# Kernel optimization log

Hardware: AMD Instinct MI355X
Metric: run time of the kernel (lower is better)

## Reference

```python
import jax, jax.numpy as jnp
import numpy as np

B, S, HID = 2, 2048, 2048
NH, NKV, HD = 16, 8, 128
GROUPS = NH // NKV
EPS = 1e-6
SCALE = HD ** -0.5
ROPE_THETA = 1000000.0


def _rope_cos_sin(seq_len, head_dim, batch):
    inv_freq = 1.0 / (ROPE_THETA ** (np.arange(0, head_dim, 2, dtype=np.float32) / head_dim))
    t = np.arange(seq_len, dtype=np.float32)
    freqs = np.outer(t, inv_freq)                      # [S, HD/2]
    emb = np.concatenate([freqs, freqs], axis=-1)      # [S, HD]
    cos = np.broadcast_to(np.cos(emb), (batch, seq_len, head_dim))
    sin = np.broadcast_to(np.sin(emb), (batch, seq_len, head_dim))
    return jnp.asarray(cos), jnp.asarray(sin)


def setup_inputs() -> dict:
    key = jax.random.key(0)
    ks = jax.random.split(key, 6)
    hidden_states = jax.random.normal(ks[0], (B, S, HID), dtype=jnp.float32)
    cos, sin = _rope_cos_sin(S, HD, B)
    w_scale = HID ** -0.5
    Wq = jax.random.normal(ks[1], (NH * HD, HID), dtype=jnp.float32) * w_scale
    Wk = jax.random.normal(ks[2], (NKV * HD, HID), dtype=jnp.float32) * w_scale
    Wv = jax.random.normal(ks[3], (NKV * HD, HID), dtype=jnp.float32) * w_scale
    Wo = jax.random.normal(ks[4], (HID, NH * HD), dtype=jnp.float32) * w_scale
    q_norm_w = jnp.ones((HD,), dtype=jnp.float32)
    k_norm_w = jnp.ones((HD,), dtype=jnp.float32)
    return {"hidden_states": hidden_states, "cos": cos, "sin": sin,
            "Wq": Wq, "Wk": Wk, "Wv": Wv, "Wo": Wo,
            "q_norm_w": q_norm_w, "k_norm_w": k_norm_w}


def _rms_norm(x, w):
    # RMSNorm over last dim (head_dim), variance computed in fp32
    var = jnp.mean(x.astype(jnp.float32) ** 2, axis=-1, keepdims=True)
    return w * (x * jax.lax.rsqrt(var + EPS).astype(x.dtype))


def _rotate_half(x):
    x1, x2 = jnp.split(x, 2, axis=-1)
    return jnp.concatenate([-x2, x1], axis=-1)


def _apply_rope(x, cos, sin):
    # x: [B, H, S, D]; cos/sin: [B, S, D] -> unsqueeze head dim
    c = cos[:, None, :, :]
    s = sin[:, None, :, :]
    return x * c + _rotate_half(x) * s


def reference(hidden_states, cos, sin, Wq, Wk, Wv, Wo, q_norm_w, k_norm_w):
    b, s, _ = hidden_states.shape
    # QKV projections (bias=False per config.attention_bias)
    q = (hidden_states @ Wq.T).reshape(b, s, NH, HD)
    k = (hidden_states @ Wk.T).reshape(b, s, NKV, HD)
    v = (hidden_states @ Wv.T).reshape(b, s, NKV, HD)
    # Per-head QK RMSNorm, then [B, H, S, D]
    q = _rms_norm(q, q_norm_w).transpose(0, 2, 1, 3)
    k = _rms_norm(k, k_norm_w).transpose(0, 2, 1, 3)
    v = v.transpose(0, 2, 1, 3)
    # RoPE
    q = _apply_rope(q, cos, sin)
    k = _apply_rope(k, cos, sin)
    # GQA: expand kv heads to match query heads
    k = jnp.repeat(k, GROUPS, axis=1)
    v = jnp.repeat(v, GROUPS, axis=1)
    # SDPA (is_causal=False, mask=None, dropout=0)
    scores = jnp.einsum('bhqd,bhkd->bhqk', q, k) * SCALE
    probs = jax.nn.softmax(scores, axis=-1)
    attn = jnp.einsum('bhqk,bhkd->bhqd', probs, v)
    attn = attn.transpose(0, 2, 1, 3).reshape(b, s, NH * HD)
    return attn @ Wo.T
```

## Files before the change

kernel.cpp:

```cpp
#include <hip/hip_runtime.h>

using short8 = __attribute__((ext_vector_type(8))) short;
using f32x4  = __attribute__((ext_vector_type(4))) float;
using u32x2  = __attribute__((ext_vector_type(2))) unsigned int;
using u32x4  = __attribute__((ext_vector_type(4))) unsigned int;

#define MFMA16(a, b, c) __builtin_amdgcn_mfma_f32_16x16x32_bf16((a), (b), (c), 0, 0, 0)

__device__ inline float bf2f(ushort v) { return __uint_as_float(((unsigned int)v) << 16); }
__device__ inline unsigned int f2bfu(float f) {
  unsigned int u = __float_as_uint(f);
  return (u + 0x7fffu + ((u >> 16) & 1u)) >> 16;
}
__device__ inline unsigned int pk2(float a, float b) { return f2bfu(a) | (f2bfu(b) << 16); }

__device__ inline void gl_lds16(const ushort* g, ushort* l) {
  __builtin_amdgcn_global_load_lds(
      (const __attribute__((address_space(1))) void*)g,
      (__attribute__((address_space(3))) void*)l, 16, 0, 0);
}

__global__ __launch_bounds__(256) void f2b8(const float* __restrict__ src,
                                            ushort* __restrict__ dst, int n) {
  int i = (blockIdx.x * 256 + threadIdx.x) * 8;
  if (i >= n) return;
  f32x4 a = *(const f32x4*)(src + i);
  f32x4 b = *(const f32x4*)(src + i + 4);
  u32x4 o;
  o[0] = pk2(a[0], a[1]); o[1] = pk2(a[2], a[3]);
  o[2] = pk2(b[0], b[1]); o[3] = pk2(b[2], b[3]);
  *(u32x4*)(dst + i) = o;
}

#define GPHASE(CB, P, STG, VMW)                                                     \
  {                                                                                 \
    if (P == 0) {                                                                   \
      _Pragma("unroll") for (int n = 0; n < 4; ++n) {                               \
        bf[n][0] = *(const short8*)&L[(CB)*32768 + bBase + n*1024 + rdoff];         \
        bf[n][1] = *(const short8*)&L[(CB)*32768 + bBase + n*1024 + (rdoff ^ 32)];  \
      }                                                                             \
    }                                                                               \
    short8 af[2][2];                                                                \
    _Pragma("unroll") for (int mi = 0; mi < 2; ++mi) {                              \
      af[mi][0] = *(const short8*)&L[(CB)*32768 + aBase + ((P)*2+mi)*1024 + rdoff];        \
      af[mi][1] = *(const short8*)&L[(CB)*32768 + aBase + ((P)*2+mi)*1024 + (rdoff ^ 32)]; \
    }                                                                               \
    STG;                                                                            \
    __builtin_amdgcn_s_barrier();                                                   \
    asm volatile("s_waitcnt lgkmcnt(0)" ::: "memory");                              \
    __builtin_amdgcn_s_setprio(1);                                                  \
    _Pragma("unroll") for (int mi = 0; mi < 2; ++mi)                                \
      _Pragma("unroll") for (int n = 0; n < 4; ++n) {                               \
        acc[(P)*2+mi][n] = MFMA16(af[mi][0], bf[n][0], acc[(P)*2+mi][n]);           \
        acc[(P)*2+mi][n] = MFMA16(af[mi][1], bf[n][1], acc[(P)*2+mi][n]);           \
      }                                                                             \
    __builtin_amdgcn_s_setprio(0);                                                  \
    VMW;                                                                            \
    __builtin_amdgcn_s_barrier();                                                   \
  }

#define VM4 asm volatile("s_waitcnt vmcnt(4)" ::: "memory")
#define NOPX (void)0

template <int OUTF32>
__global__ __launch_bounds__(512, 2) void gemm256(const ushort* __restrict__ A,
                                                  const ushort* __restrict__ B,
                                                  void* __restrict__ Cv,
                                                  int M, int N, int K) {
  __shared__ ushort L[65536];
  const int t = threadIdx.x;
  const int w = t >> 6, l = t & 63, lr = l & 15, lg = l >> 4;
  const int wr = w >> 2, wc = w & 3;
  const int m0 = blockIdx.x * 256, n0 = blockIdx.y * 256;
  const int NT = K >> 6, NI = NT >> 1;

  f32x4 acc[8][4] = {};

  const int rdoff = lr * 64 + ((lg ^ (lr & 7)) * 8);
  const int aBase = wr * 8192;
  const int bBase = 16384 + (wc >> 1) * 8192 + (wc & 1) * 4096;

  const int ch0 = w * 2, ch1 = w * 2 + 1;
  const int srow0 = ch0 * 8 + (l >> 3), srow1 = ch1 * 8 + (l >> 3);
  const int scol = ((l & 7) ^ (l >> 3)) * 8;

  auto stage_a = [&](int h, int kt, int cb) {
    int ktc = kt < NT ? kt : NT - 1;
    gl_lds16(A + (size_t)(m0 + h * 128 + srow0) * K + ktc * 64 + scol,
             (ushort*)&L[cb * 32768 + h * 8192 + ch0 * 512]);
    gl_lds16(A + (size_t)(m0 + h * 128 + srow1) * K + ktc * 64 + scol,
             (ushort*)&L[cb * 32768 + h * 8192 + ch1 * 512]);
  };
  auto stage_b = [&](int h, int kt, int cb) {
    int ktc = kt < NT ? kt : NT - 1;
    gl_lds16(B + (size_t)(n0 + h * 128 + srow0) * K + ktc * 64 + scol,
             (ushort*)&L[cb * 32768 + 16384 + h * 8192 + ch0 * 512]);
    gl_lds16(B + (size_t)(n0 + h * 128 + srow1) * K + ktc * 64 + scol,
             (ushort*)&L[cb * 32768 + 16384 + h * 8192 + ch1 * 512]);
  };

  stage_a(0, 0, 0); stage_a(1, 0, 0); stage_b(0, 0, 0); stage_b(1, 0, 0);
  stage_b(0, 1, 1); stage_b(1, 1, 1);
  VM4;
  __builtin_amdgcn_s_barrier();

  short8 bf[4][2];
  for (int I = 0; I < NI; ++I) {
    const int t1 = 2 * I + 1, t2 = 2 * I + 2, t3 = 2 * I + 3;
    GPHASE(0, 0, stage_a(0, t1, 1), NOPX)
    GPHASE(0, 1, stage_a(1, t1, 1), NOPX)
    GPHASE(0, 2, stage_b(0, t2, 0), NOPX)
    GPHASE(0, 3, stage_b(1, t2, 0), VM4)
    GPHASE(1, 0, stage_a(0, t2, 0), NOPX)
    GPHASE(1, 1, stage_a(1, t2, 0), NOPX)
    GPHASE(1, 2, stage_b(0, t3, 1), NOPX)
    GPHASE(1, 3, stage_b(1, t3, 1), VM4)
  }

  const int crow0 = m0 + wr * 128 + lg * 4;
  const int ccol = n0 + wc * 64 + lr;
  if (OUTF32) {
    float* C = (float*)Cv;
#pragma unroll
    for (int m = 0; m < 8; ++m)
#pragma unroll
      for (int n = 0; n < 4; ++n)
#pragma unroll
        for (int j = 0; j < 4; ++j)
          C[(size_t)(crow0 + m * 16 + j) * N + ccol + n * 16] = acc[m][n][j];
  } else {
    ushort* C = (ushort*)Cv;
#pragma unroll
    for (int m = 0; m < 8; ++m)
#pragma unroll
      for (int n = 0; n < 4; ++n)
#pragma unroll
        for (int j = 0; j < 4; ++j)
          C[(size_t)(crow0 + m * 16 + j) * N + ccol + n * 16] = (ushort)f2bfu(acc[m][n][j]);
  }
}

__global__ __launch_bounds__(256) void qk_norm_rope(
    const ushort* __restrict__ QKVp, const float* __restrict__ cosb,
    const float* __restrict__ sinb, const float* __restrict__ qw,
    const float* __restrict__ kw, ushort* __restrict__ Qa, ushort* __restrict__ Ka) {
  int r = blockIdx.x * 4 + (threadIdx.x >> 6);
  int i = threadIdx.x & 63;
  int b, s, srccol;
  ushort* dst;
  const float* w;
  float scale;
  if (r < 65536) {
    b = r >> 15; int rem = r & 32767; s = rem >> 4; int h = rem & 15;
    srccol = h * 128;
    dst = Qa + ((size_t)((b * 16 + h) * 2048 + s)) * 128;
    w = qw;
    scale = 0.08838834764831845f * 1.4426950408889634f;
  } else {
    int rk = r - 65536;
    b = rk >> 14; int rem = rk & 16383; s = rem >> 3; int kvh = rem & 7;
    srccol = 2048 + kvh * 128;
    dst = Ka + ((size_t)((b * 8 + kvh) * 2048 + s)) * 128;
    w = kw;
    scale = 1.0f;
  }
  const ushort* src = QKVp + ((size_t)(b * 2048 + s)) * 4096 + srccol;
  float x0 = bf2f(src[i]), x1 = bf2f(src[i + 64]);
  float ss = x0 * x0 + x1 * x1;
#pragma unroll
  for (int m = 1; m < 64; m <<= 1) ss += __shfl_xor(ss, m);
  float inv = rsqrtf(ss * (1.0f / 128.0f) + 1e-6f);
  float xn0 = x0 * inv * w[i], xn1 = x1 * inv * w[i + 64];
  const float* cp = cosb + ((size_t)(b * 2048 + s)) * 128;
  const float* sp = sinb + ((size_t)(b * 2048 + s)) * 128;
  float o0 = (xn0 * cp[i] - xn1 * sp[i]) * scale;
  float o1 = (xn1 * cp[i + 64] + xn0 * sp[i + 64]) * scale;
  dst[i] = (ushort)f2bfu(o0);
  dst[i + 64] = (ushort)f2bfu(o1);
}

__global__ __launch_bounds__(256) void v_transpose(const ushort* __restrict__ QKVp,
                                                   ushort* __restrict__ Vt) {
  __shared__ ushort tile[64][136];
  int blk = blockIdx.x;
  int st = blk & 31, kvh = (blk >> 5) & 7, b = blk >> 8;
  int t = threadIdx.x;
  int s0 = st * 64;
  {
    int r = t >> 2, cseg = (t & 3) * 32;
    const ushort* src = QKVp + ((size_t)(b * 2048 + s0 + r)) * 4096 + 3072 + kvh * 128 + cseg;
#pragma unroll
    for (int i = 0; i < 4; ++i)
      *(uint4*)&tile[r][cseg + i * 8] = *(const uint4*)(src + i * 8);
  }
  __syncthreads();
  {
    int d = t >> 1, sh = (t & 1) * 32;
    ushort* dst = Vt + ((size_t)((b * 8 + kvh) * 128 + d)) * 2048 + s0 + sh;
    ushort buf[32];
#pragma unroll
    for (int k = 0; k < 32; ++k) buf[k] = tile[sh + k][d];
#pragma unroll
    for (int i = 0; i < 4; ++i) *(uint4*)(dst + i * 8) = *(uint4*)&buf[i * 8];
  }
}

__global__ __launch_bounds__(256, 2) void attn_kernel(const ushort* __restrict__ Qa,
                                                      const ushort* __restrict__ Ka,
                                                      const ushort* __restrict__ Vt,
                                                      ushort* __restrict__ Ctx) {
  __shared__ ushort Ks[2][64 * 128];
  __shared__ ushort Vs[2][128 * 64];
  __shared__ ushort Ps[8 * 1024];
  const int bh = blockIdx.x, b = bh >> 4, h = bh & 15, kvh = h >> 1;
  const int t = threadIdx.x, w = t >> 6, l = t & 63, lr = l & 15, lg = l >> 4;
  const int q0 = blockIdx.y * 128 + w * 32;
  const ushort* Qh = Qa + ((size_t)(b * 16 + h)) * 2048 * 128;
  const ushort* Kh = Ka + ((size_t)(b * 8 + kvh)) * 2048 * 128;
  const ushort* Vh = Vt + ((size_t)(b * 8 + kvh)) * 128 * 2048;

  short8 bq[2][4];
#pragma unroll
  for (int qt = 0; qt < 2; ++qt)
#pragma unroll
    for (int dc = 0; dc < 4; ++dc)
      bq[qt][dc] = *(const short8*)&Qh[(size_t)(q0 + qt * 16 + lr) * 128 + dc * 32 + lg * 8];
  asm volatile("s_waitcnt vmcnt(0)" ::: "memory");

  f32x4 accO[8][2] = {};
  float mrun[2] = {-3.0e38f, -3.0e38f};
  float lrun[2] = {0.f, 0.f};

  auto stage = [&](int kt0, ushort* KSB, ushort* VSB) {
#pragma unroll
    for (int i = 0; i < 4; ++i) {
      const int c = w * 4 + i;
      const int krow = c * 4 + lg;
      gl_lds16(Kh + (size_t)(kt0 + krow) * 128 + (((l & 15) ^ (krow & 7)) * 8),
               KSB + c * 512);
      const int vrow = c * 8 + (l >> 3);
      gl_lds16(Vh + (size_t)vrow * 2048 + kt0 + (((l & 7) ^ ((l >> 3) & 7)) * 8),
               VSB + c * 512);
    }
  };

  auto iter = [&](int kt, const ushort* KSB, const ushort* VSB, ushort* KSN, ushort* VSN) {
    f32x4 accS[4][2] = {};
#pragma unroll
    for (int dc = 0; dc < 4; ++dc) {
      short8 ak[4];
#pragma unroll
      for (int kts = 0; kts < 4; ++kts)
        ak[kts] = *(const short8*)&KSB[(kts * 16 + lr) * 128 + ((dc * 4 + lg) ^ (lr & 7)) * 8];
#pragma unroll
      for (int kts = 0; kts < 4; ++kts)
#pragma unroll
        for (int qt = 0; qt < 2; ++qt)
          accS[kts][qt] = MFMA16(ak[kts], bq[qt][dc], accS[kts][qt]);
    }

#pragma unroll
    for (int qt = 0; qt < 2; ++qt) {
      float m0 = fmaxf(fmaxf(accS[0][qt][0], accS[0][qt][1]), fmaxf(accS[0][qt][2], accS[0][qt][3]));
      float m1 = fmaxf(fmaxf(accS[1][qt][0], accS[1][qt][1]), fmaxf(accS[1][qt][2], accS[1][qt][3]));
      float m2 = fmaxf(fmaxf(accS[2][qt][0], accS[2][qt][1]), fmaxf(accS[2][qt][2], accS[2][qt][3]));
      float m3 = fmaxf(fmaxf(accS[3][qt][0], accS[3][qt][1]), fmaxf(accS[3][qt][2], accS[3][qt][3]));
      float tm = fmaxf(fmaxf(m0, m1), fmaxf(m2, m3));
      tm = fmaxf(tm, __shfl_xor(tm, 16));
      tm = fmaxf(tm, __shfl_xor(tm, 32));
      if (!__all(tm <= mrun[qt] + 11.0f)) {
        float nm = fmaxf(mrun[qt], tm);
        float cf = __builtin_amdgcn_exp2f(mrun[qt] - nm);
#pragma unroll
        for (int dc = 0; dc < 8; ++dc) {
          accO[dc][qt][0] *= cf; accO[dc][qt][1] *= cf;
          accO[dc][qt][2] *= cf; accO[dc][qt][3] *= cf;
        }
        lrun[qt] *= cf;
        mrun[qt] = nm;
      }
      float ts = 0.f;
#pragma unroll
      for (int kts = 0; kts < 4; ++kts)
#pragma unroll
        for (int j = 0; j < 4; ++j) {
          float p = __builtin_amdgcn_exp2f(accS[kts][qt][j] - mrun[qt]);
          accS[kts][qt][j] = p;
          ts += p;
        }
      ts += __shfl_xor(ts, 16);
      ts += __shfl_xor(ts, 32);
      lrun[qt] += ts;
#pragma unroll
      for (int kts = 0; kts < 4; ++kts) {
        u32x2 pv;
        pv[0] = pk2(accS[kts][qt][0], accS[kts][qt][1]);
        pv[1] = pk2(accS[kts][qt][2], accS[kts][qt][3]);
        *(u32x2*)&Ps[(w * 2 + qt) * 1024 + lr * 64 +
                     (((kts * 2 + (lg >> 1)) ^ (lr & 7)) * 8 + (lg & 1) * 4)] = pv;
      }
    }
    asm volatile("s_waitcnt lgkmcnt(0)" ::: "memory");

    short8 bp[2][2];
#pragma unroll
    for (int qt = 0; qt < 2; ++qt)
#pragma unroll
      for (int ks = 0; ks < 2; ++ks)
        bp[qt][ks] = *(const short8*)&Ps[(w * 2 + qt) * 1024 + lr * 64 +
                                         ((ks * 4 + lg) ^ (lr & 7)) * 8];
#pragma unroll
    for (int dc = 0; dc < 8; ++dc) {
      short8 av[2];
#pragma unroll
      for (int ks = 0; ks < 2; ++ks)
        av[ks] = *(const short8*)&VSB[(dc * 16 + lr) * 64 + ((ks * 4 + lg) ^ (lr & 7)) * 8];
#pragma unroll
      for (int ks = 0; ks < 2; ++ks)
#pragma unroll
        for (int qt = 0; qt < 2; ++qt)
          accO[dc][qt] = MFMA16(av[ks], bp[qt][ks], accO[dc][qt]);
    }

    asm volatile("" ::: "memory");
    __builtin_amdgcn_s_barrier();
    if (kt + 128 <= 2048) {
      stage(kt + 128, KSN, VSN);
      asm volatile("s_waitcnt vmcnt(8)" ::: "memory");
    } else {
      asm volatile("s_waitcnt vmcnt(0)" ::: "memory");
    }
    __builtin_amdgcn_s_barrier();
  };

  stage(0, Ks[0], Vs[0]);
  stage(64, Ks[1], Vs[1]);
  asm volatile("s_waitcnt vmcnt(8)" ::: "memory");
  __builtin_amdgcn_s_barrier();

  for (int t2 = 0; t2 < 2048; t2 += 128) {
    iter(t2,      Ks[0], Vs[0], Ks[0], Vs[0]);
    iter(t2 + 64, Ks[1], Vs[1], Ks[1], Vs[1]);
  }

#pragma unroll
  for (int qt = 0; qt < 2; ++qt) {
    float inv = 1.0f / lrun[qt];
    int srow = q0 + qt * 16 + lr;
#pragma unroll
    for (int dc = 0; dc < 8; ++dc) {
      u32x2 ov;
      ov[0] = pk2(accO[dc][qt][0] * inv, accO[dc][qt][1] * inv);
      ov[1] = pk2(accO[dc][qt][2] * inv, accO[dc][qt][3] * inv);
      *(u32x2*)&Ctx[(size_t)(b * 2048 + srow) * 2048 + h * 128 + dc * 16 + lg * 4] = ov;
    }
  }
}

extern "C" void kernel_launch(void* const* d_in, const int* in_sizes, int n_in,
                              void* d_out, int out_size, void* d_ws, size_t ws_size,
                              hipStream_t stream) {
  const float* hidden = (const float*)d_in[0];
  const float* cosb   = (const float*)d_in[1];
  const float* sinb   = (const float*)d_in[2];
  const float* Wq     = (const float*)d_in[3];
  const float* Wk     = (const float*)d_in[4];
  const float* Wv     = (const float*)d_in[5];
  const float* Wo     = (const float*)d_in[6];
  const float* qw     = (const float*)d_in[7];
  const float* kw     = (const float*)d_in[8];

  char* ws = (char*)d_ws;
  ushort* Xb    = (ushort*)ws; ws += (size_t)4096 * 2048 * 2;
  ushort* Wcomb = (ushort*)ws; ws += (size_t)4096 * 2048 * 2;
  ushort* Wob   = (ushort*)ws; ws += (size_t)2048 * 2048 * 2;
  ushort* QKVp  = (ushort*)ws; ws += (size_t)4096 * 4096 * 2;
  ushort* Qa    = (ushort*)ws; ws += (size_t)2 * 16 * 2048 * 128 * 2;
  ushort* Ka    = (ushort*)ws; ws += (size_t)2 * 8 * 2048 * 128 * 2;
  ushort* Vt    = (ushort*)ws; ws += (size_t)2 * 8 * 2048 * 128 * 2;
  ushort* Ctx   = (ushort*)ws; ws += (size_t)4096 * 2048 * 2;

  f2b8<<<4096, 256, 0, stream>>>(hidden, Xb, 8388608);
  f2b8<<<2048, 256, 0, stream>>>(Wq, Wcomb, 4194304);
  f2b8<<<1024, 256, 0, stream>>>(Wk, Wcomb + 4194304, 2097152);
  f2b8<<<1024, 256, 0, stream>>>(Wv, Wcomb + 6291456, 2097152);
  f2b8<<<2048, 256, 0, stream>>>(Wo, Wob, 4194304);

  gemm256<0><<<dim3(16, 16), 512, 0, stream>>>(Xb, Wcomb, (void*)QKVp, 4096, 4096, 2048);

  qk_norm_rope<<<24576, 256, 0, stream>>>(QKVp, cosb, sinb, qw, kw, Qa, Ka);
  v_transpose<<<512, 256, 0, stream>>>(QKVp, Vt);

  attn_kernel<<<dim3(32, 16), 256, 0, stream>>>(Qa, Ka, Vt, Ctx);

  gemm256<1><<<dim3(16, 8), 512, 0, stream>>>(Ctx, Wob, d_out, 4096, 2048, 2048);
}
```

Before: 362.3 us.

## Retile attention to 8 waves, add 128-row output GEMM, fuse weight casts

The attention kernel now runs 512 threads per block, with each wave owning 16 query rows instead of 32. It also uses s_setprio around its MFMA sections and packs bf16 with the hardware v_cvt_pk_bf16_f32 instruction. A new gemm128 kernel with 128x256 tiles replaces the 256-tile output projection, doubling the grid to fill more CUs. The four weight-conversion launches are merged into one kernel. Together these aim to raise occupancy, improve CU utilisation on the output GEMM, and cut launch overhead, at the cost of more K/V LDS traffic per query row.

After: 358.8 us. About the same (-1.0%).

```diff
diff --git a/kernel.cpp b/kernel.cpp
--- a/kernel.cpp
+++ b/kernel.cpp
@@ -13,6 +13,11 @@
   return (u + 0x7fffu + ((u >> 16) & 1u)) >> 16;
 }
 __device__ inline unsigned int pk2(float a, float b) { return f2bfu(a) | (f2bfu(b) << 16); }
+__device__ inline unsigned int pk2hw(float lo, float hi) {
+  unsigned int r;
+  asm("v_cvt_pk_bf16_f32 %0, %1, %2" : "=v"(r) : "v"(lo), "v"(hi));
+  return r;
+}
 
 __device__ inline void gl_lds16(const ushort* g, ushort* l) {
   __builtin_amdgcn_global_load_lds(
@@ -24,6 +29,27 @@
                                             ushort* __restrict__ dst, int n) {
   int i = (blockIdx.x * 256 + threadIdx.x) * 8;
   if (i >= n) return;
+  f32x4 a = *(const f32x4*)(src + i);
+  f32x4 b = *(const f32x4*)(src + i + 4);
+  u32x4 o;
+  o[0] = pk2(a[0], a[1]); o[1] = pk2(a[2], a[3]);
+  o[2] = pk2(b[0], b[1]); o[3] = pk2(b[2], b[3]);
+  *(u32x4*)(dst + i) = o;
+}
+
+__global__ __launch_bounds__(256) void wconv(const float* __restrict__ Wq,
+                                             const float* __restrict__ Wk,
+                                             const float* __restrict__ Wv,
+                                             const float* __restrict__ Wo,
+                                             ushort* __restrict__ Wcomb,
+                                             ushort* __restrict__ Wob) {
+  int blk = blockIdx.x;
+  const float* src; ushort* dst; int off;
+  if (blk < 2048)      { src = Wq; dst = Wcomb;           off = blk * 2048; }
+  else if (blk < 3072) { src = Wk; dst = Wcomb + 4194304; off = (blk - 2048) * 2048; }
+  else if (blk < 4096) { src = Wv; dst = Wcomb + 6291456; off = (blk - 3072) * 2048; }
+  else                 { src = Wo; dst = Wob;             off = (blk - 4096) * 2048; }
+  int i = off + threadIdx.x * 8;
   f32x4 a = *(const f32x4*)(src + i);
   f32x4 b = *(const f32x4*)(src + i + 4);
   u32x4 o;
@@ -140,6 +166,92 @@
   }
 }
 
+#define GP128(CB, P, STG, VMW)                                                      \
+  {                                                                                 \
+    if (P == 0) {                                                                   \
+      _Pragma("unroll") for (int n = 0; n < 4; ++n) {                               \
+        bf[n][0] = *(const short8*)&L[(CB)*24576 + bBase + n*1024 + rdoff];         \
+        bf[n][1] = *(const short8*)&L[(CB)*24576 + bBase + n*1024 + (rdoff ^ 32)];  \
+      }                                                                             \
+    }                                                                               \
+    short8 af0 = *(const short8*)&L[(CB)*24576 + aBase + (P)*1024 + rdoff];         \
+    short8 af1 = *(const short8*)&L[(CB)*24576 + aBase + (P)*1024 + (rdoff ^ 32)];  \
+    STG;                                                                            \
+    __builtin_amdgcn_s_barrier();                                                   \
+    asm volatile("s_waitcnt lgkmcnt(0)" ::: "memory");                              \
+    __builtin_amdgcn_s_setprio(1);                                                  \
+    _Pragma("unroll") for (int n = 0; n < 4; ++n) {                                 \
+      acc[(P)][n] = MFMA16(af0, bf[n][0], acc[(P)][n]);                             \
+      acc[(P)][n] = MFMA16(af1, bf[n][1], acc[(P)][n]);                             \
+    }                                                                               \
+    __builtin_amdgcn_s_setprio(0);                                                  \
+    VMW;                                                                            \
+    __builtin_amdgcn_s_barrier();                                                   \
+  }
+
+__global__ __launch_bounds__(512, 2) void gemm128(const ushort* __restrict__ A,
+                                                  const ushort* __restrict__ B,
+                                                  float* __restrict__ C,
+                                                  int M, int N, int K) {
+  __shared__ ushort L[49152];
+  const int t = threadIdx.x;
+  const int w = t >> 6, l = t & 63, lr = l & 15, lg = l >> 4;
+  const int wr = w >> 2, wc = w & 3;
+  const int m0 = blockIdx.x * 128, n0 = blockIdx.y * 256;
+  const int NT = K >> 6, NI = NT >> 1;
+
+  f32x4 acc[4][4] = {};
+
+  const int rdoff = lr * 64 + ((lg ^ (lr & 7)) * 8);
+  const int aBase = wr * 4096;
+  const int bBase = 8192 + wc * 4096;
+  const int scol = ((l & 7) ^ (l >> 3)) * 8;
+
+  auto stage_a_h = [&](int h, int kt, int cb) {
+    int ktc = kt < NT ? kt : NT - 1;
+    int ch = h * 8 + w;
+    gl_lds16(A + (size_t)(m0 + ch * 8 + (l >> 3)) * K + ktc * 64 + scol,
+             (ushort*)&L[cb * 24576 + ch * 512]);
+  };
+  auto stage_b_h = [&](int h, int kt, int cb) {
+    int ktc = kt < NT ? kt : NT - 1;
+    int c0 = h * 16 + w * 2, c1 = c0 + 1;
+    gl_lds16(B + (size_t)(n0 + c0 * 8 + (l >> 3)) * K + ktc * 64 + scol,
+             (ushort*)&L[cb * 24576 + 8192 + c0 * 512]);
+    gl_lds16(B + (size_t)(n0 + c1 * 8 + (l >> 3)) * K + ktc * 64 + scol,
+             (ushort*)&L[cb * 24576 + 8192 + c1 * 512]);
+  };
+
+  stage_a_h(0, 0, 0); stage_a_h(1, 0, 0);
+  stage_b_h(0, 0, 0); stage_b_h(1, 0, 0);
+  stage_b_h(0, 1, 1); stage_b_h(1, 1, 1);
+  VM4;
+  __builtin_amdgcn_s_barrier();
+
+  short8 bf[4][2];
+  for (int I = 0; I < NI; ++I) {
+    const int t1 = 2 * I + 1, t2 = 2 * I + 2, t3 = 2 * I + 3;
+    GP128(0, 0, stage_a_h(0, t1, 1), NOPX)
+    GP128(0, 1, stage_a_h(1, t1, 1), NOPX)
+    GP128(0, 2, stage_b_h(0, t2, 0), NOPX)
+    GP128(0, 3, stage_b_h(1, t2, 0), VM4)
+    GP128(1, 0, stage_a_h(0, t2, 0), NOPX)
+    GP128(1, 1, stage_a_h(1, t2, 0), NOPX)
+    GP128(1, 2, stage_b_h(0, t3, 1), NOPX)
+    GP128(1, 3, stage_b_h(1, t3, 1), VM4)
+  }
+
+  const int crow0 = m0 + wr * 64 + lg * 4;
+  const int ccol = n0 + wc * 64 + lr;
+#pragma unroll
+  for (int m = 0; m < 4; ++m)
+#pragma unroll
+    for (int n = 0; n < 4; ++n)
+#pragma unroll
+      for (int j = 0; j < 4; ++j)
+        C[(size_t)(crow0 + m * 16 + j) * N + ccol + n * 16] = acc[m][n][j];
+}
+
 __global__ __launch_bounds__(256) void qk_norm_rope(
     const ushort* __restrict__ QKVp, const float* __restrict__ cosb,
     const float* __restrict__ sinb, const float* __restrict__ qw,
@@ -205,7 +317,7 @@
   }
 }
 
-__global__ __launch_bounds__(256, 2) void attn_kernel(const ushort* __restrict__ Qa,
+__global__ __launch_bounds__(512, 4) void attn_kernel(const ushort* __restrict__ Qa,
                                                       const ushort* __restrict__ Ka,
                                                       const ushort* __restrict__ Vt,
                                                       ushort* __restrict__ Ctx) {
@@ -214,38 +326,34 @@
   __shared__ ushort Ps[8 * 1024];
   const int bh = blockIdx.x, b = bh >> 4, h = bh & 15, kvh = h >> 1;
   const int t = threadIdx.x, w = t >> 6, l = t & 63, lr = l & 15, lg = l >> 4;
-  const int q0 = blockIdx.y * 128 + w * 32;
+  const int q0 = blockIdx.y * 128 + w * 16;
   const ushort* Qh = Qa + ((size_t)(b * 16 + h)) * 2048 * 128;
   const ushort* Kh = Ka + ((size_t)(b * 8 + kvh)) * 2048 * 128;
   const ushort* Vh = Vt + ((size_t)(b * 8 + kvh)) * 128 * 2048;
 
-  short8 bq[2][4];
-#pragma unroll
-  for (int qt = 0; qt < 2; ++qt)
-#pragma unroll
-    for (int dc = 0; dc < 4; ++dc)
-      bq[qt][dc] = *(const short8*)&Qh[(size_t)(q0 + qt * 16 + lr) * 128 + dc * 32 + lg * 8];
+  short8 bq[4];
+#pragma unroll
+  for (int dc = 0; dc < 4; ++dc)
+    bq[dc] = *(const short8*)&Qh[(size_t)(q0 + lr) * 128 + dc * 32 + lg * 8];
   asm volatile("s_waitcnt vmcnt(0)" ::: "memory");
 
-  f32x4 accO[8][2] = {};
-  float mrun[2] = {-3.0e38f, -3.0e38f};
-  float lrun[2] = {0.f, 0.f};
+  f32x4 accO[8] = {};
+  float mrun = -3.0e38f, lrun = 0.f;
 
   auto stage = [&](int kt0, ushort* KSB, ushort* VSB) {
 #pragma unroll
-    for (int i = 0; i < 4; ++i) {
-      const int c = w * 4 + i;
+    for (int i = 0; i < 2; ++i) {
+      const int c = w * 2 + i;
       const int krow = c * 4 + lg;
-      gl_lds16(Kh + (size_t)(kt0 + krow) * 128 + (((l & 15) ^ (krow & 7)) * 8),
-               KSB + c * 512);
+      gl_lds16(Kh + (size_t)(kt0 + krow) * 128 + ((lr ^ (krow & 7)) * 8), KSB + c * 512);
       const int vrow = c * 8 + (l >> 3);
-      gl_lds16(Vh + (size_t)vrow * 2048 + kt0 + (((l & 7) ^ ((l >> 3) & 7)) * 8),
-               VSB + c * 512);
-    }
-  };
-
-  auto iter = [&](int kt, const ushort* KSB, const ushort* VSB, ushort* KSN, ushort* VSN) {
-    f32x4 accS[4][2] = {};
+      gl_lds16(Vh + (size_t)vrow * 2048 + kt0 + (((l & 7) ^ ((l >> 3) & 7)) * 8), VSB + c * 512);
+    }
+  };
+
+  auto iter = [&](int kt, ushort* KSB, ushort* VSB) {
+    f32x4 accS[4] = {};
+    __builtin_amdgcn_s_setprio(1);
 #pragma unroll
     for (int dc = 0; dc < 4; ++dc) {
       short8 ak[4];
@@ -254,61 +362,57 @@
         ak[kts] = *(const short8*)&KSB[(kts * 16 + lr) * 128 + ((dc * 4 + lg) ^ (lr & 7)) * 8];
 #pragma unroll
       for (int kts = 0; kts < 4; ++kts)
-#pragma unroll
-        for (int qt = 0; qt < 2; ++qt)
-          accS[kts][qt] = MFMA16(ak[kts], bq[qt][dc], accS[kts][qt]);
-    }
-
-#pragma unroll
-    for (int qt = 0; qt < 2; ++qt) {
-      float m0 = fmaxf(fmaxf(accS[0][qt][0], accS[0][qt][1]), fmaxf(accS[0][qt][2], accS[0][qt][3]));
-      float m1 = fmaxf(fmaxf(accS[1][qt][0], accS[1][qt][1]), fmaxf(accS[1][qt][2], accS[1][qt][3]));
-      float m2 = fmaxf(fmaxf(accS[2][qt][0], accS[2][qt][1]), fmaxf(accS[2][qt][2], accS[2][qt][3]));
-      float m3 = fmaxf(fmaxf(accS[3][qt][0], accS[3][qt][1]), fmaxf(accS[3][qt][2], accS[3][qt][3]));
+        accS[kts] = MFMA16(ak[kts], bq[dc], accS[kts]);
+    }
+    __builtin_amdgcn_s_setprio(0);
+
+    {
+      float m0 = fmaxf(fmaxf(accS[0][0], accS[0][1]), fmaxf(accS[0][2], accS[0][3]));
+      float m1 = fmaxf(fmaxf(accS[1][0], accS[1][1]), fmaxf(accS[1][2], accS[1][3]));
+      float m2 = fmaxf(fmaxf(accS[2][0], accS[2][1]), fmaxf(accS[2][2], accS[2][3]));
+      float m3 = fmaxf(fmaxf(accS[3][0], accS[3][1]), fmaxf(accS[3][2], accS[3][3]));
       float tm = fmaxf(fmaxf(m0, m1), fmaxf(m2, m3));
       tm = fmaxf(tm, __shfl_xor(tm, 16));
       tm = fmaxf(tm, __shfl_xor(tm, 32));
-      if (!__all(tm <= mrun[qt] + 11.0f)) {
-        float nm = fmaxf(mrun[qt], tm);
-        float cf = __builtin_amdgcn_exp2f(mrun[qt] - nm);
+      if (!__all(tm <= mrun + 11.0f)) {
+        float nm = fmaxf(mrun, tm);
+        float cf = __builtin_amdgcn_exp2f(mrun - nm);
 #pragma unroll
         for (int dc = 0; dc < 8; ++dc) {
-          accO[dc][qt][0] *= cf; accO[dc][qt][1] *= cf;
-          accO[dc][qt][2] *= cf; accO[dc][qt][3] *= cf;
+          accO[dc][0] *= cf; accO[dc][1] *= cf;
+          accO[dc][2] *= cf; accO[dc][3] *= cf;
         }
-        lrun[qt] *= cf;
-        mrun[qt] = nm;
+        lrun *= cf;
+        mrun = nm;
       }
       float ts = 0.f;
 #pragma unroll
       for (int kts = 0; kts < 4; ++kts)
 #pragma unroll
         for (int j = 0; j < 4; ++j) {
-          float p = __builtin_amdgcn_exp2f(accS[kts][qt][j] - mrun[qt]);
-          accS[kts][qt][j] = p;
+          float p = __builtin_amdgcn_exp2f(accS[kts][j] - mrun);
+          accS[kts][j] = p;
           ts += p;
         }
       ts += __shfl_xor(ts, 16);
       ts += __shfl_xor(ts, 32);
-      lrun[qt] += ts;
+      lrun += ts;
 #pragma unroll
       for (int kts = 0; kts < 4; ++kts) {
         u32x2 pv;
-        pv[0] = pk2(accS[kts][qt][0], accS[kts][qt][1]);
-        pv[1] = pk2(accS[kts][qt][2], accS[kts][qt][3]);
-        *(u32x2*)&Ps[(w * 2 + qt) * 1024 + lr * 64 +
+        pv[0] = pk2hw(accS[kts][0], accS[kts][1]);
+        pv[1] = pk2hw(accS[kts][2], accS[kts][3]);
+        *(u32x2*)&Ps[w * 1024 + lr * 64 +
                      (((kts * 2 + (lg >> 1)) ^ (lr & 7)) * 8 + (lg & 1) * 4)] = pv;
       }
     }
     asm volatile("s_waitcnt lgkmcnt(0)" ::: "memory");
 
-    short8 bp[2][2];
-#pragma unroll
-    for (int qt = 0; qt < 2; ++qt)
-#pragma unroll
-      for (int ks = 0; ks < 2; ++ks)
-        bp[qt][ks] = *(const short8*)&Ps[(w * 2 + qt) * 1024 + lr * 64 +
-                                         ((ks * 4 + lg) ^ (lr & 7)) * 8];
+    short8 bp[2];
+#pragma unroll
+    for (int ks = 0; ks < 2; ++ks)
+      bp[ks] = *(const short8*)&Ps[w * 1024 + lr * 64 + ((ks * 4 + lg) ^ (lr & 7)) * 8];
+    __builtin_amdgcn_s_setprio(1);
 #pragma unroll
     for (int dc = 0; dc < 8; ++dc) {
       short8 av[2];
@@ -317,16 +421,15 @@
         av[ks] = *(const short8*)&VSB[(dc * 16 + lr) * 64 + ((ks * 4 + lg) ^ (lr & 7)) * 8];
 #pragma unroll
       for (int ks = 0; ks < 2; ++ks)
-#pragma unroll
-        for (int qt = 0; qt < 2; ++qt)
-          accO[dc][qt] = MFMA16(av[ks], bp[qt][ks], accO[dc][qt]);
-    }
+        accO[dc] = MFMA16(av[ks], bp[ks], accO[dc]);
+    }
+    __builtin_amdgcn_s_setprio(0);
 
     asm volatile("" ::: "memory");
     __builtin_amdgcn_s_barrier();
-    if (kt + 128 <= 2048) {
-      stage(kt + 128, KSN, VSN);
-      asm volatile("s_waitcnt vmcnt(8)" ::: "memory");
+    if (kt + 128 < 2048) {
+      stage(kt + 128, KSB, VSB);
+      asm volatile("s_waitcnt vmcnt(4)" ::: "memory");
     } else {
       asm volatile("s_waitcnt vmcnt(0)" ::: "memory");
     }
@@ -335,23 +438,22 @@
 
   stage(0, Ks[0], Vs[0]);
   stage(64, Ks[1], Vs[1]);
-  asm volatile("s_waitcnt vmcnt(8)" ::: "memory");
+  asm volatile("s_waitcnt vmcnt(4)" ::: "memory");
   __builtin_amdgcn_s_barrier();
 
   for (int t2 = 0; t2 < 2048; t2 += 128) {
-    iter(t2,      Ks[0], Vs[0], Ks[0], Vs[0]);
-    iter(t2 + 64, Ks[1], Vs[1], Ks[1], Vs[1]);
-  }
-
-#pragma unroll
-  for (int qt = 0; qt < 2; ++qt) {
-    float inv = 1.0f / lrun[qt];
-    int srow = q0 + qt * 16 + lr;
+    iter(t2,      Ks[0], Vs[0]);
+    iter(t2 + 64, Ks[1], Vs[1]);
+  }
+
+  {
+    float inv = 1.0f / lrun;
+    int srow = q0 + lr;
 #pragma unroll
     for (int dc = 0; dc < 8; ++dc) {
       u32x2 ov;
-      ov[0] = pk2(accO[dc][qt][0] * inv, accO[dc][qt][1] * inv);
-      ov[1] = pk2(accO[dc][qt][2] * inv, accO[dc][qt][3] * inv);
+      ov[0] = pk2hw(accO[dc][0] * inv, accO[dc][1] * inv);
+      ov[1] = pk2hw(accO[dc][2] * inv, accO[dc][3] * inv);
       *(u32x2*)&Ctx[(size_t)(b * 2048 + srow) * 2048 + h * 128 + dc * 16 + lg * 4] = ov;
     }
   }
@@ -381,17 +483,14 @@
   ushort* Ctx   = (ushort*)ws; ws += (size_t)4096 * 2048 * 2;
 
   f2b8<<<4096, 256, 0, stream>>>(hidden, Xb, 8388608);
-  f2b8<<<2048, 256, 0, stream>>>(Wq, Wcomb, 4194304);
-  f2b8<<<1024, 256, 0, stream>>>(Wk, Wcomb + 4194304, 2097152);
-  f2b8<<<1024, 256, 0, stream>>>(Wv, Wcomb + 6291456, 2097152);
-  f2b8<<<2048, 256, 0, stream>>>(Wo, Wob, 4194304);
+  wconv<<<6144, 256, 0, stream>>>(Wq, Wk, Wv, Wo, Wcomb, Wob);
 
   gemm256<0><<<dim3(16, 16), 512, 0, stream>>>(Xb, Wcomb, (void*)QKVp, 4096, 4096, 2048);
 
   qk_norm_rope<<<24576, 256, 0, stream>>>(QKVp, cosb, sinb, qw, kw, Qa, Ka);
   v_transpose<<<512, 256, 0, stream>>>(QKVp, Vt);
 
-  attn_kernel<<<dim3(32, 16), 256, 0, stream>>>(Qa, Ka, Vt, Ctx);
-
-  gemm256<1><<<dim3(16, 8), 512, 0, stream>>>(Ctx, Wob, d_out, 4096, 2048, 2048);
-}
+  attn_kernel<<<dim3(32, 16), 512, 0, stream>>>(Qa, Ka, Vt, Ctx);
+
+  gemm128<<<dim3(32, 8), 512, 0, stream>>>(Ctx, Wob, (float*)d_out, 4096, 2048, 2048);
+}
```
